# Optimization experiments

Measured on AMD Instinct MI355X. Metric: run time of the kernel, lower is better.

The kernel has to match this reference:

```python
import jax, jax.numpy as jnp
import numpy as np

N = 100000
E = 1000000
IN_C, HID, OUT_C = 64, 64, 40


def setup_inputs() -> dict:
    key = jax.random.key(0)
    ks = jax.random.split(key, 12)
    x = jax.random.normal(ks[0], (N, IN_C), dtype=jnp.float32)
    edge_index = jax.random.randint(ks[1], (2, E), 0, N, dtype=jnp.int64)

    def glorot(k, fan_in, fan_out):
        s = (6.0 / (fan_in + fan_out)) ** 0.5
        return jax.random.uniform(k, (fan_in, fan_out), jnp.float32, -s, s)

    return {
        "x": x,
        "edge_index": edge_index,
        "W1": glorot(ks[2], IN_C, HID), "b1": jnp.zeros((HID,), jnp.float32),
        "W2": glorot(ks[3], HID, HID), "b2": jnp.zeros((HID,), jnp.float32),
        "Wm1": glorot(ks[4], HID, HID), "bm1": jnp.zeros((HID,), jnp.float32),
        "Wm2": glorot(ks[5], HID, OUT_C), "bm2": jnp.zeros((OUT_C,), jnp.float32),
    }


def _gcn_conv(h_in, W, b, src, dst, deg_inv_sqrt):
    # PyG GCNConv: x' = D^{-1/2} (A + I) D^{-1/2} (x W) + b, self-loops added.
    h = h_in @ W                                        # [N, F]
    norm = deg_inv_sqrt[src] * deg_inv_sqrt[dst]        # [E]
    msg = h[src] * norm[:, None]                        # gather + scale
    agg = jax.ops.segment_sum(msg, dst, num_segments=N)  # scatter-add
    # self-loop contribution: deg_i^{-1/2} * deg_i^{-1/2} * h_i
    agg = agg + h * (deg_inv_sqrt * deg_inv_sqrt)[:, None]
    return agg + b


def reference(x, edge_index, W1, b1, W2, b2, Wm1, bm1, Wm2, bm2):
    src, dst = edge_index[0], edge_index[1]
    deg = jax.ops.segment_sum(jnp.ones((E,), jnp.float32), dst, num_segments=N) + 1.0
    deg_inv_sqrt = jax.lax.rsqrt(deg)

    h = _gcn_conv(x, W1, b1, src, dst, deg_inv_sqrt)
    h = jax.nn.relu(h)
    h = _gcn_conv(h, W2, b2, src, dst, deg_inv_sqrt)  # no relu after last conv

    h = jax.nn.relu(h @ Wm1 + bm1)
    out = h @ Wm2 + bm2
    return out
```

## Files before the change

kernel.cpp:

```cpp
#include <hip/hip_runtime.h>
#include <hip/hip_bf16.h>
#include <hip/hip_fp16.h>


namespace {

constexpr int N_NODES = 100000;
constexpr int N_EDGES = 1000000;
constexpr int NBUCK = (N_NODES + 511) / 512;
constexpr int CAP = 8192;
constexpr int EPB_A = 2048;

__global__ __launch_bounds__(256) void bucket_kernel(const void* __restrict__ ei,
                                                     int* __restrict__ bucketCnt,
                                                     unsigned* __restrict__ tmp) {
  __shared__ int hist[NBUCK];
  __shared__ int basePB[NBUCK];
  __shared__ int cur[NBUCK];
  __shared__ int sflag;
  int t = threadIdx.x;
  if (t < NBUCK) { hist[t] = 0; cur[t] = 0; }
  if (t == 0) sflag = 0;
  __syncthreads();

  int e0 = blockIdx.x * EPB_A;
  const unsigned* w = (const unsigned*)ei;
  unsigned any = 0;
#pragma unroll
  for (int s = 0; s < 2; s++) {
    int e = e0 + s * 256 + t;
    if (e < N_EDGES) any |= w[2 * e + 1];
  }
  if (any) sflag = 1;
  __syncthreads();
  int is32 = sflag;

  unsigned wreg[8];
  int breg[8];
#pragma unroll
  for (int k = 0; k < 8; k++) {
    int e = e0 + k * 256 + t;
    breg[k] = -1;
    if (e < N_EDGES) {
      int s, d;
      if (is32) {
        const int* p = (const int*)ei;
        s = p[e]; d = p[N_EDGES + e];
      } else {
        const long long* p = (const long long*)ei;
        s = (int)p[e]; d = (int)p[N_EDGES + e];
      }
      wreg[k] = ((unsigned)s << 9) | (unsigned)(d & 511);
      breg[k] = d >> 9;
      atomicAdd(&hist[breg[k]], 1);
    }
  }
  __syncthreads();
  if (t < NBUCK) basePB[t] = hist[t] ? atomicAdd(&bucketCnt[t], hist[t]) : 0;
  __syncthreads();
#pragma unroll
  for (int k = 0; k < 8; k++) {
    if (breg[k] >= 0) {
      int r = atomicAdd(&cur[breg[k]], 1);
      tmp[(size_t)breg[k] * CAP + basePB[breg[k]] + r] = wreg[k];
    }
  }
}

__global__ __launch_bounds__(512) void csr_kernel(const unsigned* __restrict__ tmp,
                                                  const int* __restrict__ bucketCnt,
                                                  int* __restrict__ col,
                                                  int* __restrict__ row_start,
                                                  int* __restrict__ row_end,
                                                  float* __restrict__ dinv) {
  __shared__ int sc[512];
  __shared__ int hist[512];
  __shared__ unsigned stage[CAP];
  int b = blockIdx.x, t = threadIdx.x;
  int myCnt = bucketCnt[b];
  int base = b * CAP;

  hist[t] = 0;
  __syncthreads();
  for (int i = t; i < myCnt; i += 512) {
    unsigned w = tmp[(size_t)base + i];
    stage[i] = w;
    atomicAdd(&hist[w & 511u], 1);
  }
  __syncthreads();

  int deg = hist[t];
  int pdeg = (deg + 7) & ~7;
  sc[t] = pdeg;
  __syncthreads();
#pragma unroll
  for (int off = 1; off < 512; off <<= 1) {
    int u = (t >= off) ? sc[t - off] : 0;
    __syncthreads();
    sc[t] += u;
    __syncthreads();
  }
  int pexcl = sc[t] - pdeg;
  int d = b * 512 + t;
  if (d < N_NODES) {
    row_start[d] = base + pexcl;
    row_end[d] = base + pexcl + pdeg;
    dinv[d] = rsqrtf((float)deg + 1.0f);
  }
  __syncthreads();
  hist[t] = pexcl;
  __syncthreads();
  for (int i = t; i < myCnt; i += 512) {
    unsigned w = stage[i];
    int pos = atomicAdd(&hist[w & 511u], 1);
    col[base + pos] = (int)(w >> 9);
  }
  for (int j = deg; j < pdeg; j++) col[base + pexcl + j] = N_NODES;
}

__device__ inline uint4 pack_half8(const float* v) {
  __half2 h0 = __floats2half2_rn(v[0], v[1]);
  __half2 h1 = __floats2half2_rn(v[2], v[3]);
  __half2 h2 = __floats2half2_rn(v[4], v[5]);
  __half2 h3 = __floats2half2_rn(v[6], v[7]);
  uint4 u;
  u.x = *(unsigned*)&h0; u.y = *(unsigned*)&h1;
  u.z = *(unsigned*)&h2; u.w = *(unsigned*)&h3;
  return u;
}

__global__ __launch_bounds__(256) void gemm_g_kernel(const float* __restrict__ A,
                                                     const float* __restrict__ W,
                                                     const float* __restrict__ dinv,
                                                     __half* __restrict__ g,
                                                     int reluIn) {
  __shared__ float Ws[64 * 64];
  int t = threadIdx.x;
  if (blockIdx.x == 0 && t < 32) ((float*)(g + (size_t)N_NODES * 64))[t] = 0.f;
  for (int i = t; i < 64 * 64 / 4; i += 256) ((float4*)Ws)[i] = ((const float4*)W)[i];
  __syncthreads();

  int rg = t >> 3, cg = t & 7;
  int r0 = blockIdx.x * 128 + rg * 4;
  int c0 = cg * 8;

  float acc[4][8];
#pragma unroll
  for (int i = 0; i < 4; i++)
#pragma unroll
    for (int j = 0; j < 8; j++) acc[i][j] = 0.f;

  const float4* A4 = (const float4*)A;
  for (int kk = 0; kk < 16; kk++) {
    float4 a[4];
#pragma unroll
    for (int i = 0; i < 4; i++) {
      int r = r0 + i;
      float4 v = (r < N_NODES) ? A4[(size_t)r * 16 + kk] : make_float4(0.f, 0.f, 0.f, 0.f);
      if (reluIn) {
        v.x = fmaxf(v.x, 0.f); v.y = fmaxf(v.y, 0.f);
        v.z = fmaxf(v.z, 0.f); v.w = fmaxf(v.w, 0.f);
      }
      a[i] = v;
    }
#pragma unroll
    for (int q = 0; q < 4; q++) {
      int k = kk * 4 + q;
      float w[8];
#pragma unroll
      for (int j = 0; j < 2; j++) *(float4*)&w[4 * j] = *(const float4*)&Ws[k * 64 + c0 + 4 * j];
#pragma unroll
      for (int i = 0; i < 4; i++) {
        float av = q == 0 ? a[i].x : q == 1 ? a[i].y : q == 2 ? a[i].z : a[i].w;
#pragma unroll
        for (int j = 0; j < 8; j++) acc[i][j] = fmaf(av, w[j], acc[i][j]);
      }
    }
  }
#pragma unroll
  for (int i = 0; i < 4; i++) {
    int r = r0 + i;
    if (r < N_NODES) {
      float s = dinv[r];
#pragma unroll
      for (int j = 0; j < 8; j++) acc[i][j] *= s;
      *(uint4*)(g + (size_t)r * 64 + c0) = pack_half8(acc[i]);
    }
  }
}

__global__ __launch_bounds__(256) void aggregate_kernel(const __half* __restrict__ g,
                                                        const int* __restrict__ col,
                                                        const int* __restrict__ row_start,
                                                        const int* __restrict__ row_end,
                                                        const float* __restrict__ dinv,
                                                        const float* __restrict__ bias,
                                                        float* __restrict__ out) {
  int wave = threadIdx.x >> 6;
  int lane = threadIdx.x & 63;
  int half = lane >> 5;
  int sub = lane & 31;
  int d = blockIdx.x * 8 + wave * 2 + half;

  const __half2* g2 = (const __half2*)g;
  int e0 = row_start[d];
  int len = row_end[d] - e0;

  float2 a0 = __half22float2(g2[(size_t)d * 32 + sub]);
  float2 a1 = {0.f, 0.f}, a2 = {0.f, 0.f}, a3 = {0.f, 0.f};
  float2 a4 = {0.f, 0.f}, a5 = {0.f, 0.f}, a6 = {0.f, 0.f}, a7 = {0.f, 0.f};

  for (int i = 0; i < len; i += 8) {
    int4 ca = *(const int4*)(col + e0 + i);
    int4 cb = *(const int4*)(col + e0 + i + 4);
    float2 h0 = __half22float2(g2[(size_t)ca.x * 32 + sub]);
    float2 h1 = __half22float2(g2[(size_t)ca.y * 32 + sub]);
    float2 h2 = __half22float2(g2[(size_t)ca.z * 32 + sub]);
    float2 h3 = __half22float2(g2[(size_t)ca.w * 32 + sub]);
    float2 h4 = __half22float2(g2[(size_t)cb.x * 32 + sub]);
    float2 h5 = __half22float2(g2[(size_t)cb.y * 32 + sub]);
    float2 h6 = __half22float2(g2[(size_t)cb.z * 32 + sub]);
    float2 h7 = __half22float2(g2[(size_t)cb.w * 32 + sub]);
    a0.x += h0.x; a0.y += h0.y; a1.x += h1.x; a1.y += h1.y;
    a2.x += h2.x; a2.y += h2.y; a3.x += h3.x; a3.y += h3.y;
    a4.x += h4.x; a4.y += h4.y; a5.x += h5.x; a5.y += h5.y;
    a6.x += h6.x; a6.y += h6.y; a7.x += h7.x; a7.y += h7.y;
  }
  float rx = ((a0.x + a1.x) + (a2.x + a3.x)) + ((a4.x + a5.x) + (a6.x + a7.x));
  float ry = ((a0.y + a1.y) + (a2.y + a3.y)) + ((a4.y + a5.y) + (a6.y + a7.y));
  float dv = dinv[d];
  float2 bv = ((const float2*)bias)[sub];
  float2 o;
  o.x = fmaf(rx, dv, bv.x);
  o.y = fmaf(ry, dv, bv.y);
  ((float2*)out)[(size_t)d * 32 + sub] = o;
}

template <int F>
__global__ __launch_bounds__(256) void gemm_kernel(const float* __restrict__ A, const float* __restrict__ W,
                                                   const float* __restrict__ bias, float* __restrict__ C,
                                                   int n, int reluIn, int reluOut) {
  constexpr int CPT = F / 8;
  __shared__ float Ws[64 * F];
  int t = threadIdx.x;
  for (int i = t; i < 64 * F / 4; i += 256) ((float4*)Ws)[i] = ((const float4*)W)[i];
  __syncthreads();

  int rg = t >> 3, cg = t & 7;
  int r0 = blockIdx.x * 128 + rg * 4;
  int c0 = cg * CPT;

  float acc[4][CPT];
#pragma unroll
  for (int i = 0; i < 4; i++)
#pragma unroll
    for (int j = 0; j < CPT; j++) acc[i][j] = 0.f;

  const float4* A4 = (const float4*)A;
  for (int kk = 0; kk < 16; kk++) {
    float4 a[4];
#pragma unroll
    for (int i = 0; i < 4; i++) {
      int r = r0 + i;
      float4 v = (r < n) ? A4[(size_t)r * 16 + kk] : make_float4(0.f, 0.f, 0.f, 0.f);
      if (reluIn) {
        v.x = fmaxf(v.x, 0.f); v.y = fmaxf(v.y, 0.f);
        v.z = fmaxf(v.z, 0.f); v.w = fmaxf(v.w, 0.f);
      }
      a[i] = v;
    }
#pragma unroll
    for (int q = 0; q < 4; q++) {
      int k = kk * 4 + q;
      float w[CPT];
      if constexpr (CPT % 4 == 0) {
#pragma unroll
        for (int j = 0; j < CPT / 4; j++)
          *(float4*)&w[4 * j] = *(const float4*)&Ws[k * F + c0 + 4 * j];
      } else {
#pragma unroll
        for (int j = 0; j < CPT; j++) w[j] = Ws[k * F + c0 + j];
      }
#pragma unroll
      for (int i = 0; i < 4; i++) {
        float av = q == 0 ? a[i].x : q == 1 ? a[i].y : q == 2 ? a[i].z : a[i].w;
#pragma unroll
        for (int j = 0; j < CPT; j++) acc[i][j] = fmaf(av, w[j], acc[i][j]);
      }
    }
  }

  float bv[CPT];
#pragma unroll
  for (int j = 0; j < CPT; j++) bv[j] = bias ? bias[c0 + j] : 0.f;
#pragma unroll
  for (int i = 0; i < 4; i++) {
    int r = r0 + i;
    if (r < n) {
      float* crow = C + (size_t)r * F + c0;
#pragma unroll
      for (int j = 0; j < CPT; j++) {
        float v = acc[i][j] + bv[j];
        if (reluOut) v = fmaxf(v, 0.f);
        crow[j] = v;
      }
    }
  }
}

}

extern "C" void kernel_launch(void* const* d_in, const int* in_sizes, int n_in,
                              void* d_out, int out_size, void* d_ws, size_t ws_size,
                              hipStream_t stream) {
  const float* x   = (const float*)d_in[0];
  const void*  ei  = d_in[1];
  const float* W1  = (const float*)d_in[2];
  const float* b1  = (const float*)d_in[3];
  const float* W2  = (const float*)d_in[4];
  const float* b2  = (const float*)d_in[5];
  const float* Wm1 = (const float*)d_in[6];
  const float* bm1 = (const float*)d_in[7];
  const float* Wm2 = (const float*)d_in[8];
  const float* bm2 = (const float*)d_in[9];
  float* out = (float*)d_out;

  char* ws = (char*)d_ws;
  size_t off = 0;
  auto alloc = [&](size_t bytes) -> void* {
    void* p = ws + off;
    off = (off + bytes + 511) & ~(size_t)511;
    return p;
  };
  int*      bucketCnt = (int*)     alloc((size_t)NBUCK * 4);
  unsigned* tmp       = (unsigned*)alloc((size_t)NBUCK * CAP * 4);
  int*      colA      = (int*)     alloc((size_t)NBUCK * CAP * 4);
  int*      rowS      = (int*)     alloc((size_t)N_NODES * 4);
  int*      rowE      = (int*)     alloc((size_t)N_NODES * 4);
  float*    dinv      = (float*)   alloc((size_t)N_NODES * 4);
  __half*   g1        = (__half*)  alloc((size_t)(N_NODES + 1) * 64 * 2);
  float*    hA        = (float*)   alloc((size_t)N_NODES * 64 * 4);
  float*    hB        = (float*)   alloc((size_t)N_NODES * 64 * 4);
  (void)ws_size; (void)in_sizes; (void)n_in; (void)out_size;

  dim3 b256(256);
  int gGemm = (N_NODES + 127) / 128;
  int gAgg  = N_NODES / 8;
  int gBkt  = (N_EDGES + EPB_A - 1) / EPB_A;

  hipMemsetAsync(bucketCnt, 0, (size_t)NBUCK * 4, stream);
  bucket_kernel<<<gBkt, b256, 0, stream>>>(ei, bucketCnt, tmp);
  csr_kernel<<<NBUCK, dim3(512), 0, stream>>>(tmp, bucketCnt, colA, rowS, rowE, dinv);

  gemm_g_kernel<<<gGemm, b256, 0, stream>>>(x, W1, dinv, g1, 0);
  aggregate_kernel<<<gAgg, b256, 0, stream>>>(g1, colA, rowS, rowE, dinv, b1, hB);

  gemm_g_kernel<<<gGemm, b256, 0, stream>>>(hB, W2, dinv, g1, 1);
  aggregate_kernel<<<gAgg, b256, 0, stream>>>(g1, colA, rowS, rowE, dinv, b2, hB);

  gemm_kernel<64><<<gGemm, b256, 0, stream>>>(hB, Wm1, bm1, hA, N_NODES, 0, 1);
  gemm_kernel<40><<<gGemm, b256, 0, stream>>>(hA, Wm2, bm2, out, N_NODES, 0, 0);
}
```

Baseline: 253.7 us.

## Shrink CSR buckets and sort nodes by degree class for balanced aggregation

Destination buckets shrink from 512 to 128 nodes, giving more, smaller CSR blocks with less shared staging each. The CSR kernel also builds a per-bucket permutation that groups nodes by padded-degree class. The aggregate kernel reads node ids through this permutation, so the two nodes in a wave and the waves in a block see similar edge counts, which reduces divergence. The cost is an extra indirection in the aggregate kernel, scattered output writes, and the risk of CAP=2560 overflowing for heavily loaded buckets.

```diff
diff --git a/kernel.cpp b/kernel.cpp
--- a/kernel.cpp
+++ b/kernel.cpp
@@ -7,8 +7,9 @@
 
 constexpr int N_NODES = 100000;
 constexpr int N_EDGES = 1000000;
-constexpr int NBUCK = (N_NODES + 511) / 512;
-constexpr int CAP = 8192;
+constexpr int BN = 128;
+constexpr int NBUCK = (N_NODES + BN - 1) / BN;
+constexpr int CAP = 2560;
 constexpr int EPB_A = 2048;
 
 __global__ __launch_bounds__(256) void bucket_kernel(const void* __restrict__ ei,
@@ -19,7 +20,7 @@
   __shared__ int cur[NBUCK];
   __shared__ int sflag;
   int t = threadIdx.x;
-  if (t < NBUCK) { hist[t] = 0; cur[t] = 0; }
+  for (int i = t; i < NBUCK; i += 256) { hist[i] = 0; cur[i] = 0; }
   if (t == 0) sflag = 0;
   __syncthreads();
 
@@ -50,13 +51,14 @@
         const long long* p = (const long long*)ei;
         s = (int)p[e]; d = (int)p[N_EDGES + e];
       }
-      wreg[k] = ((unsigned)s << 9) | (unsigned)(d & 511);
-      breg[k] = d >> 9;
+      wreg[k] = ((unsigned)s << 7) | (unsigned)(d & 127);
+      breg[k] = d >> 7;
       atomicAdd(&hist[breg[k]], 1);
     }
   }
   __syncthreads();
-  if (t < NBUCK) basePB[t] = hist[t] ? atomicAdd(&bucketCnt[t], hist[t]) : 0;
+  for (int i = t; i < NBUCK; i += 256)
+    basePB[i] = hist[i] ? atomicAdd(&bucketCnt[i], hist[i]) : 0;
   __syncthreads();
 #pragma unroll
   for (int k = 0; k < 8; k++) {
@@ -67,55 +69,71 @@
   }
 }
 
-__global__ __launch_bounds__(512) void csr_kernel(const unsigned* __restrict__ tmp,
+__global__ __launch_bounds__(256) void csr_kernel(const unsigned* __restrict__ tmp,
                                                   const int* __restrict__ bucketCnt,
                                                   int* __restrict__ col,
                                                   int* __restrict__ row_start,
                                                   int* __restrict__ row_end,
+                                                  int* __restrict__ perm,
                                                   float* __restrict__ dinv) {
-  __shared__ int sc[512];
-  __shared__ int hist[512];
+  __shared__ int sc[BN];
+  __shared__ int hist[BN];
+  __shared__ int chist[33];
+  __shared__ int cbase[33];
   __shared__ unsigned stage[CAP];
   int b = blockIdx.x, t = threadIdx.x;
   int myCnt = bucketCnt[b];
   int base = b * CAP;
-
-  hist[t] = 0;
-  __syncthreads();
-  for (int i = t; i < myCnt; i += 512) {
-    unsigned w = tmp[(size_t)base + i];
+  int nb = min(BN, N_NODES - b * BN);
+
+  if (t < BN) hist[t] = 0;
+  if (t < 33) chist[t] = 0;
+  __syncthreads();
+  for (int i = t; i < myCnt; i += 256) {
+    unsigned w = tmp[base + i];
     stage[i] = w;
-    atomicAdd(&hist[w & 511u], 1);
-  }
-  __syncthreads();
-
-  int deg = hist[t];
+    atomicAdd(&hist[w & 127u], 1);
+  }
+  __syncthreads();
+
+  int deg = (t < BN) ? hist[t] : 0;
   int pdeg = (deg + 7) & ~7;
-  sc[t] = pdeg;
-  __syncthreads();
-#pragma unroll
-  for (int off = 1; off < 512; off <<= 1) {
-    int u = (t >= off) ? sc[t - off] : 0;
+  if (t < BN) sc[t] = pdeg;
+  __syncthreads();
+  for (int off = 1; off < BN; off <<= 1) {
+    int u = (t >= off && t < BN) ? sc[t - off] : 0;
     __syncthreads();
-    sc[t] += u;
+    if (t < BN) sc[t] += u;
     __syncthreads();
   }
-  int pexcl = sc[t] - pdeg;
-  int d = b * 512 + t;
-  if (d < N_NODES) {
+  int pexcl = (t < BN) ? sc[t] - pdeg : 0;
+  int d = b * BN + t;
+  if (t < nb) {
     row_start[d] = base + pexcl;
     row_end[d] = base + pexcl + pdeg;
     dinv[d] = rsqrtf((float)deg + 1.0f);
   }
   __syncthreads();
-  hist[t] = pexcl;
-  __syncthreads();
-  for (int i = t; i < myCnt; i += 512) {
+  if (t < BN) hist[t] = pexcl;
+  __syncthreads();
+  for (int i = t; i < myCnt; i += 256) {
     unsigned w = stage[i];
-    int pos = atomicAdd(&hist[w & 511u], 1);
-    col[base + pos] = (int)(w >> 9);
-  }
-  for (int j = deg; j < pdeg; j++) col[base + pexcl + j] = N_NODES;
+    int pos = atomicAdd(&hist[w & 127u], 1);
+    col[base + pos] = (int)(w >> 7);
+  }
+  if (t < nb)
+    for (int j = deg; j < pdeg; j++) col[base + pexcl + j] = N_NODES;
+
+  int cls = min(pdeg >> 3, 32);
+  int idx = 0;
+  if (t < nb) idx = atomicAdd(&chist[cls], 1);
+  __syncthreads();
+  if (t == 0) {
+    int run = 0;
+    for (int c = 0; c <= 32; c++) { cbase[c] = run; run += chist[c]; }
+  }
+  __syncthreads();
+  if (t < nb) perm[b * BN + cbase[cls] + idx] = d;
 }
 
 __device__ inline uint4 pack_half8(const float* v) {
@@ -193,6 +211,7 @@
                                                         const int* __restrict__ col,
                                                         const int* __restrict__ row_start,
                                                         const int* __restrict__ row_end,
+                                                        const int* __restrict__ perm,
                                                         const float* __restrict__ dinv,
                                                         const float* __restrict__ bias,
                                                         float* __restrict__ out) {
@@ -200,7 +219,7 @@
   int lane = threadIdx.x & 63;
   int half = lane >> 5;
   int sub = lane & 31;
-  int d = blockIdx.x * 8 + wave * 2 + half;
+  int d = perm[blockIdx.x * 8 + wave * 2 + half];
 
   const __half2* g2 = (const __half2*)g;
   int e0 = row_start[d];
@@ -337,6 +356,7 @@
   int*      colA      = (int*)     alloc((size_t)NBUCK * CAP * 4);
   int*      rowS      = (int*)     alloc((size_t)N_NODES * 4);
   int*      rowE      = (int*)     alloc((size_t)N_NODES * 4);
+  int*      perm      = (int*)     alloc((size_t)N_NODES * 4);
   float*    dinv      = (float*)   alloc((size_t)N_NODES * 4);
   __half*   g1        = (__half*)  alloc((size_t)(N_NODES + 1) * 64 * 2);
   float*    hA        = (float*)   alloc((size_t)N_NODES * 64 * 4);
@@ -350,13 +370,13 @@
 
   hipMemsetAsync(bucketCnt, 0, (size_t)NBUCK * 4, stream);
   bucket_kernel<<<gBkt, b256, 0, stream>>>(ei, bucketCnt, tmp);
-  csr_kernel<<<NBUCK, dim3(512), 0, stream>>>(tmp, bucketCnt, colA, rowS, rowE, dinv);
+  csr_kernel<<<NBUCK, dim3(256), 0, stream>>>(tmp, bucketCnt, colA, rowS, rowE, perm, dinv);
 
   gemm_g_kernel<<<gGemm, b256, 0, stream>>>(x, W1, dinv, g1, 0);
-  aggregate_kernel<<<gAgg, b256, 0, stream>>>(g1, colA, rowS, rowE, dinv, b1, hB);
+  aggregate_kernel<<<gAgg, b256, 0, stream>>>(g1, colA, rowS, rowE, perm, dinv, b1, hB);
 
   gemm_g_kernel<<<gGemm, b256, 0, stream>>>(hB, W2, dinv, g1, 1);
-  aggregate_kernel<<<gAgg, b256, 0, stream>>>(g1, colA, rowS, rowE, dinv, b2, hB);
+  aggregate_kernel<<<gAgg, b256, 0, stream>>>(g1, colA, rowS, rowE, perm, dinv, b2, hB);
 
   gemm_kernel<64><<<gGemm, b256, 0, stream>>>(hB, Wm1, bm1, hA, N_NODES, 0, 1);
   gemm_kernel<40><<<gGemm, b256, 0, stream>>>(hA, Wm2, bm2, out, N_NODES, 0, 0);
```

After: 268.5 us. 5.8% more time.
